# Kernel tuning notes

Hardware: AMD Instinct MI355X
Metric: run time of the kernel (lower is better)

Reference implementation:

```python
import jax, jax.numpy as jnp
import numpy as np

B, S, R, H, NH, HD = 32, 1026, 256, 1024, 16, 64

def setup_inputs() -> dict:
    key = jax.random.key(0)
    ks = jax.random.split(key, 8)
    sc = 0.02
    return {
        "q_low": jax.random.normal(ks[0], (B, S, R), jnp.float32),
        "k_low": jax.random.normal(ks[1], (B, S, R), jnp.float32),
        "v_low": jax.random.normal(ks[2], (B, S, R), jnp.float32),
        "Wq": jax.random.normal(ks[3], (R, H), jnp.float32) * sc,
        "bq": jnp.zeros((H,), jnp.float32),
        "Wk": jax.random.normal(ks[4], (R, H), jnp.float32) * sc,
        "bk": jnp.zeros((H,), jnp.float32),
        "Wv": jax.random.normal(ks[5], (R, H), jnp.float32) * sc,
        "bv": jnp.zeros((H,), jnp.float32),
        "Wo_down": jax.random.normal(ks[6], (H, R), jnp.float32) * sc,
    }

def reference(q_low, k_low, v_low, Wq, bq, Wk, bk, Wv, bv, Wo_down):
    # Up-project low-rank activations to full Q, K, V: [B,S,R] @ [R,H] -> [B,S,H]
    q = q_low @ Wq + bq
    k = k_low @ Wk + bk
    v = v_low @ Wv + bv
    # split heads: [B,S,NH,HD] -> [B,NH,S,HD]
    def split(x):
        return x.reshape(B, S, NH, HD).transpose(0, 2, 1, 3)
    qh, kh, vh = split(q), split(k), split(v)
    scores = jnp.einsum('bhqd,bhkd->bhqk', qh, kh) / jnp.sqrt(jnp.float32(HD))
    probs = jax.nn.softmax(scores, axis=-1)  # dropout p=0
    ctx = jnp.einsum('bhqk,bhkd->bhqd', probs, vh)
    ctx = ctx.transpose(0, 2, 1, 3).reshape(B, S, H)
    # Down-project with low-rank activation (gelu)
    out_low = jax.nn.gelu(ctx @ Wo_down, approximate=False)
    return out_low
```

## Files before the change

kernel.cpp:

```cpp
#include <hip/hip_runtime.h>
#include <hip/hip_bf16.h>
#include <math.h>

using short8   = __attribute__((ext_vector_type(8))) short;
using floatx4  = __attribute__((ext_vector_type(4))) float;
using floatx16 = __attribute__((ext_vector_type(16))) float;

#define B_N  32
#define S_N  1026
#define R_N  256
#define H_N  1024
#define NH_N 16
#define HD_N 64
#define SP_N 1088
#define KTILES 17

__device__ __forceinline__ float bf2f(__hip_bfloat16 x) { return __bfloat162float(x); }
__device__ __forceinline__ __hip_bfloat16 f2bf(float x) { return __float2bfloat16(x); }

__device__ __forceinline__ float fast_exp2(float x) {
#if __has_builtin(__builtin_amdgcn_exp2f)
    return __builtin_amdgcn_exp2f(x);
#else
    return exp2f(x);
#endif
}

__device__ __forceinline__ unsigned cvtpk(float lo, float hi_) {
    unsigned r;
    asm("v_cvt_pk_bf16_f32 %0, %1, %2" : "=v"(r) : "v"(lo), "v"(hi_));
    return r;
}

__device__ __forceinline__ void gl_lds16(const void* g, void* l) {
    __builtin_amdgcn_global_load_lds(
        (const __attribute__((address_space(1))) unsigned int*)g,
        (__attribute__((address_space(3))) unsigned int*)l, 16, 0, 0);
}

__device__ __forceinline__ int xcd_swz(int o, int nwg) {
    return ((nwg & 7) == 0) ? ((o & 7) * (nwg >> 3) + (o >> 3)) : o;
}

__device__ __forceinline__ short8 cvt8(const float* __restrict__ p) {
    floatx4 a = *(const floatx4*)p;
    floatx4 b = *(const floatx4*)(p + 4);
    short8 o;
    __hip_bfloat16* op = (__hip_bfloat16*)&o;
    op[0] = f2bf(a[0]); op[1] = f2bf(a[1]); op[2] = f2bf(a[2]); op[3] = f2bf(a[3]);
    op[4] = f2bf(b[0]); op[5] = f2bf(b[1]); op[6] = f2bf(b[2]); op[7] = f2bf(b[3]);
    return o;
}

__global__ __launch_bounds__(256) void transpose3_kernel(
    const float* __restrict__ a, const float* __restrict__ b, const float* __restrict__ c,
    __hip_bfloat16* __restrict__ oa, __hip_bfloat16* __restrict__ ob,
    __hip_bfloat16* __restrict__ oc, int K, int N) {
    __shared__ __hip_bfloat16 t[32][33];
    const float* in = (blockIdx.z == 0) ? a : (blockIdx.z == 1) ? b : c;
    __hip_bfloat16* out = (blockIdx.z == 0) ? oa : (blockIdx.z == 1) ? ob : oc;
    const int k0 = blockIdx.x * 32, n0 = blockIdx.y * 32;
    const int tx = threadIdx.x & 31, ty = threadIdx.x >> 5;
#pragma unroll
    for (int j = 0; j < 32; j += 8)
        t[ty + j][tx] = f2bf(in[(size_t)(k0 + ty + j) * N + n0 + tx]);
    __syncthreads();
#pragma unroll
    for (int j = 0; j < 32; j += 8)
        out[(size_t)(n0 + ty + j) * K + k0 + tx] = t[tx][ty + j];
}

__global__ __launch_bounds__(256) void transpose_kernel(const float* __restrict__ in,
                                                        __hip_bfloat16* __restrict__ out,
                                                        int K, int N) {
    __shared__ __hip_bfloat16 t[32][33];
    const int k0 = blockIdx.x * 32, n0 = blockIdx.y * 32;
    const int tx = threadIdx.x & 31, ty = threadIdx.x >> 5;
#pragma unroll
    for (int j = 0; j < 32; j += 8)
        t[ty + j][tx] = f2bf(in[(size_t)(k0 + ty + j) * N + n0 + tx]);
    __syncthreads();
#pragma unroll
    for (int j = 0; j < 32; j += 8)
        out[(size_t)(n0 + ty + j) * K + k0 + tx] = t[tx][ty + j];
}

__global__ __launch_bounds__(256) void cvtx_kernel(
    const float* __restrict__ q, const float* __restrict__ k, const float* __restrict__ v,
    __hip_bfloat16* __restrict__ oq, __hip_bfloat16* __restrict__ ok,
    __hip_bfloat16* __restrict__ ov, int n8) {
    int idx = blockIdx.x * 256 + threadIdx.x;
    if (idx >= n8) return;
    const float* s = (blockIdx.y == 0) ? q : (blockIdx.y == 1) ? k : v;
    __hip_bfloat16* d = (blockIdx.y == 0) ? oq : (blockIdx.y == 1) ? ok : ov;
    *(short8*)(d + (size_t)idx * 8) = cvt8(s + (size_t)idx * 8);
}

__global__ void padv_kernel(__hip_bfloat16* __restrict__ Vt, int total) {
    int idx = blockIdx.x * 256 + threadIdx.x;
    if (idx < total) {
        int p  = idx % (SP_N - S_N);
        int rd = idx / (SP_N - S_N);
        Vt[(size_t)rd * SP_N + S_N + p] = f2bf(0.f);
    }
}

__global__ __launch_bounds__(256) void qkvproj_kernel(
    const __hip_bfloat16* __restrict__ Xq, const __hip_bfloat16* __restrict__ Xk,
    const __hip_bfloat16* __restrict__ Xv,
    const __hip_bfloat16* __restrict__ WqT, const __hip_bfloat16* __restrict__ WkT,
    const __hip_bfloat16* __restrict__ WvT,
    const float* __restrict__ bq, const float* __restrict__ bk,
    const float* __restrict__ bv,
    __hip_bfloat16* __restrict__ Qc, __hip_bfloat16* __restrict__ Kc,
    __hip_bfloat16* __restrict__ Vc, int Mc, float qscale) {
    __shared__ __hip_bfloat16 As[2][128][64];
    __shared__ __hip_bfloat16 Bs[2][128][64];

    const int nx = gridDim.x;
    const int nwg = nx * 8 * 3;
    const int o = blockIdx.x + nx * (blockIdx.y + 8 * blockIdx.z);
    const int tlin = xcd_swz(o, nwg);
    const int ty = tlin & 7;
    const int rest = tlin >> 3;
    const int tx = rest % nx, tz = rest / nx;

    const __hip_bfloat16* X  = (tz == 0) ? Xq  : (tz == 1) ? Xk  : Xv;
    const __hip_bfloat16* WT = (tz == 0) ? WqT : (tz == 1) ? WkT : WvT;
    const float* bias        = (tz == 0) ? bq  : (tz == 1) ? bk  : bv;
    __hip_bfloat16* out      = (tz == 0) ? Qc  : (tz == 1) ? Kc  : Vc;
    const float oscale = (tz == 0) ? qscale : 1.0f;
    const int mode = (tz == 2);

    const int tid  = threadIdx.x;
    const int wave = tid >> 6, lane = tid & 63;
    const int quad = lane >> 4, l16 = lane & 15;
    const int tm = tx * 128, tn = ty * 128;
    const int mw = (wave >> 1) * 64, nw = (wave & 1) * 64;
    const int lr = lane >> 3;
    const int sc = (lane & 7) ^ lr;

    floatx4 acc[4][4] = {};

    auto stage = [&](int bb, int kk) {
#pragma unroll
        for (int s8 = 0; s8 < 4; ++s8) {
            int row = wave * 32 + s8 * 8;
            int gm = tm + row + lr; if (gm >= Mc) gm = Mc - 1;
            gl_lds16(X + (size_t)gm * R_N + kk + sc * 8, &As[bb][row][0]);
            gl_lds16(WT + (size_t)(tn + row + lr) * R_N + kk + sc * 8, &Bs[bb][row][0]);
        }
    };

    stage(0, 0);
    __syncthreads();

    for (int t = 0; t < R_N / 64; ++t) {
        const int bb = t & 1;
        if (t + 1 < R_N / 64) stage(bb ^ 1, (t + 1) * 64);
        short8 af[4][2], bfr[4][2];
#pragma unroll
        for (int mb = 0; mb < 4; ++mb) {
            int row = mw + mb * 16 + l16;
            const char* rp = (const char*)&As[bb][row][0];
#pragma unroll
            for (int k2 = 0; k2 < 2; ++k2)
                af[mb][k2] = *(const short8*)(rp + ((((k2 * 4 + quad)) ^ (row & 7)) << 4));
        }
#pragma unroll
        for (int nb = 0; nb < 4; ++nb) {
            int row = nw + nb * 16 + l16;
            const char* rp = (const char*)&Bs[bb][row][0];
#pragma unroll
            for (int k2 = 0; k2 < 2; ++k2)
                bfr[nb][k2] = *(const short8*)(rp + ((((k2 * 4 + quad)) ^ (row & 7)) << 4));
        }
        if (mode == 0) {
#pragma unroll
            for (int mb = 0; mb < 4; ++mb)
#pragma unroll
                for (int nb = 0; nb < 4; ++nb) {
                    acc[mb][nb] = __builtin_amdgcn_mfma_f32_16x16x32_bf16(af[mb][0], bfr[nb][0], acc[mb][nb], 0, 0, 0);
                    acc[mb][nb] = __builtin_amdgcn_mfma_f32_16x16x32_bf16(af[mb][1], bfr[nb][1], acc[mb][nb], 0, 0, 0);
                }
        } else {
#pragma unroll
            for (int mb = 0; mb < 4; ++mb)
#pragma unroll
                for (int nb = 0; nb < 4; ++nb) {
                    acc[mb][nb] = __builtin_amdgcn_mfma_f32_16x16x32_bf16(bfr[nb][0], af[mb][0], acc[mb][nb], 0, 0, 0);
                    acc[mb][nb] = __builtin_amdgcn_mfma_f32_16x16x32_bf16(bfr[nb][1], af[mb][1], acc[mb][nb], 0, 0, 0);
                }
        }
        __syncthreads();
    }

#pragma unroll
    for (int mb = 0; mb < 4; ++mb)
#pragma unroll
        for (int nb = 0; nb < 4; ++nb)
#pragma unroll
            for (int r = 0; r < 4; ++r) {
                int m, n;
                if (mode == 0) { m = tm + mw + mb * 16 + quad * 4 + r; n = tn + nw + nb * 16 + l16; }
                else           { n = tn + nw + nb * 16 + quad * 4 + r; m = tm + mw + mb * 16 + l16; }
                if (m >= Mc) continue;
                float v = oscale * (acc[mb][nb][r] + bias[n]);
                int bl = m / S_N, s = m - bl * S_N;
                int h = n >> 6, d = n & 63;
                size_t off = (mode == 0)
                    ? ((size_t)((bl * NH_N + h) * S_N + s)) * HD_N + d
                    : ((size_t)((bl * NH_N + h) * HD_N + d)) * SP_N + s;
                out[off] = f2bf(v);
            }
}

__global__ __launch_bounds__(256, 3) void attn_kernel(
    const __hip_bfloat16* __restrict__ Qh,
    const __hip_bfloat16* __restrict__ Kh,
    const __hip_bfloat16* __restrict__ Vt,
    __hip_bfloat16* __restrict__ ctx) {
    __shared__ __hip_bfloat16 Kl[2][64][64];
    __shared__ __hip_bfloat16 Vl[2][64][64];

    const int ny = gridDim.y;
    const int nwg = gridDim.x * ny;
    const int o = blockIdx.x + gridDim.x * blockIdx.y;
    const int tlin = xcd_swz(o, nwg);
    const int bh = tlin / ny;
    const int q0 = (tlin % ny) * 128;

    const int tid = threadIdx.x;
    const int wave = tid >> 6, lane = tid & 63;
    const int c = lane & 31, hi = lane >> 5, c7 = c & 7;
    const size_t base  = (size_t)bh * S_N * HD_N;
    const size_t vbase = (size_t)bh * HD_N * SP_N;

    const int lr = lane >> 3;
    const int sc = (lane & 7) ^ lr;

    short8 qf[4];
    {
        int qrow = q0 + wave * 32 + c;
        if (qrow > S_N - 1) qrow = S_N - 1;
        const __hip_bfloat16* qp = Qh + base + (size_t)qrow * HD_N + hi * 8;
#pragma unroll
        for (int i = 0; i < 4; ++i) qf[i] = *(const short8*)(qp + 16 * i);
    }

    floatx16 oacc[2] = {};
    float lsum = 0.f;

    auto stage = [&](int bb, int kt) {
#pragma unroll
        for (int j = 0; j < 2; ++j) {
            int r = 16 * wave + 8 * j + lr;
            int krow = kt + r;
            if (krow > S_N - 1) krow = S_N - 1;
            gl_lds16(Kh + base + (size_t)krow * HD_N + sc * 8,
                     &Kl[bb][16 * wave + 8 * j][0]);
            gl_lds16(Vt + vbase + (size_t)r * SP_N + kt + sc * 8,
                     &Vl[bb][16 * wave + 8 * j][0]);
        }
    };

    stage(0, 0);
    __syncthreads();

    int bb = 0;
    for (int t = 0; t < KTILES; ++t) {
        const int kt = t * 64;
        if (t + 1 < KTILES) stage(bb ^ 1, kt + 64);
        const bool last = (kt + 64 > S_N);

        short8 pa[2][2];
#pragma unroll
        for (int sub = 0; sub < 2; ++sub) {
            floatx16 sacc = {};
            __builtin_amdgcn_s_setprio(1);
#pragma unroll
            for (int i = 0; i < 4; ++i) {
                short8 kf = *(const short8*)&Kl[bb][32 * sub + c][(((2 * i + hi) ^ c7) << 3)];
                sacc = __builtin_amdgcn_mfma_f32_32x32x16_bf16(kf, qf[i], sacc, 0, 0, 0);
            }
            __builtin_amdgcn_s_setprio(0);
            float ps[16];
            if (!last) {
#pragma unroll
                for (int r = 0; r < 16; ++r) ps[r] = fast_exp2(sacc[r]);
            } else {
#pragma unroll
                for (int r = 0; r < 16; ++r) {
                    int key = kt + 32 * sub + (r & 3) + 8 * (r >> 2) + 4 * hi;
                    ps[r] = (key < S_N) ? fast_exp2(sacc[r]) : 0.f;
                }
            }
#pragma unroll
            for (int r = 0; r < 16; ++r) lsum += ps[r];
#pragma unroll
            for (int step = 0; step < 2; ++step) {
                unsigned w0 = cvtpk(ps[8 * step + 0], ps[8 * step + 1]);
                unsigned w1 = cvtpk(ps[8 * step + 2], ps[8 * step + 3]);
                unsigned w2 = cvtpk(ps[8 * step + 4], ps[8 * step + 5]);
                unsigned w3 = cvtpk(ps[8 * step + 6], ps[8 * step + 7]);
                asm("v_permlane32_swap_b32 %0, %1" : "+v"(w0), "+v"(w2));
                asm("v_permlane32_swap_b32 %0, %1" : "+v"(w1), "+v"(w3));
                union { unsigned u[4]; short8 s; } fu;
                fu.u[0] = w0; fu.u[1] = w1; fu.u[2] = w2; fu.u[3] = w3;
                pa[sub][step] = fu.s;
            }
        }

        __builtin_amdgcn_s_setprio(1);
#pragma unroll
        for (int db = 0; db < 2; ++db)
#pragma unroll
            for (int sub = 0; sub < 2; ++sub)
#pragma unroll
                for (int step = 0; step < 2; ++step) {
                    short8 vf = *(const short8*)
                        &Vl[bb][32 * db + c][((((sub * 2 + step) * 2 + hi) ^ c7) << 3)];
                    oacc[db] = __builtin_amdgcn_mfma_f32_32x32x16_bf16(pa[sub][step], vf, oacc[db], 0, 0, 0);
                }
        __builtin_amdgcn_s_setprio(0);

        __syncthreads();
        bb ^= 1;
    }

    lsum += __shfl_xor(lsum, 32);
    float rs = 1.0f / lsum;

    const int bl = bh / NH_N, h = bh - bl * NH_N;
    const int srow0 = q0 + wave * 32;
#pragma unroll
    for (int r = 0; r < 16; ++r) {
        int q = (r & 3) + 8 * (r >> 2) + 4 * hi;
        float rr = __shfl(rs, q, 32);
        int s = srow0 + q;
        if (s < S_N) {
            size_t o2 = ((size_t)(bl * S_N + s)) * H_N + h * HD_N + c;
            ctx[o2]      = f2bf(oacc[0][r] * rr);
            ctx[o2 + 32] = f2bf(oacc[1][r] * rr);
        }
    }
}

__global__ __launch_bounds__(256) void dproj_kernel(
    const __hip_bfloat16* __restrict__ X,
    const __hip_bfloat16* __restrict__ WT,
    float* __restrict__ out,
    int Mc) {
    __shared__ __hip_bfloat16 As[2][64][64];
    __shared__ __hip_bfloat16 Bs[2][128][64];

    const int tx = blockIdx.x, ty = blockIdx.y;

    const int tid  = threadIdx.x;
    const int wave = tid >> 6, lane = tid & 63;
    const int quad = lane >> 4, l16 = lane & 15;
    const int tm = tx * 64, tn = ty * 128;
    const int mw = (wave >> 1) * 32, nw = (wave & 1) * 64;
    const int lr = lane >> 3;
    const int sc = (lane & 7) ^ lr;

    floatx4 acc[2][4] = {};

    auto stage = [&](int bb, int kk) {
#pragma unroll
        for (int s8 = 0; s8 < 2; ++s8) {
            int row = wave * 16 + s8 * 8;
            int gm = tm + row + lr; if (gm >= Mc) gm = Mc - 1;
            gl_lds16(X + (size_t)gm * H_N + kk + sc * 8, &As[bb][row][0]);
        }
#pragma unroll
        for (int s8 = 0; s8 < 4; ++s8) {
            int row = wave * 32 + s8 * 8;
            gl_lds16(WT + (size_t)(tn + row + lr) * H_N + kk + sc * 8, &Bs[bb][row][0]);
        }
    };

    stage(0, 0);
    __syncthreads();

    for (int t = 0; t < H_N / 64; ++t) {
        const int bb = t & 1;
        if (t + 1 < H_N / 64) stage(bb ^ 1, (t + 1) * 64);
        short8 af[2][2], bfr[4][2];
#pragma unroll
        for (int mb = 0; mb < 2; ++mb) {
            int row = mw + mb * 16 + l16;
            const char* rp = (const char*)&As[bb][row][0];
#pragma unroll
            for (int k2 = 0; k2 < 2; ++k2)
                af[mb][k2] = *(const short8*)(rp + ((((k2 * 4 + quad)) ^ (row & 7)) << 4));
        }
#pragma unroll
        for (int nb = 0; nb < 4; ++nb) {
            int row = nw + nb * 16 + l16;
            const char* rp = (const char*)&Bs[bb][row][0];
#pragma unroll
            for (int k2 = 0; k2 < 2; ++k2)
                bfr[nb][k2] = *(const short8*)(rp + ((((k2 * 4 + quad)) ^ (row & 7)) << 4));
        }
#pragma unroll
        for (int mb = 0; mb < 2; ++mb)
#pragma unroll
            for (int nb = 0; nb < 4; ++nb) {
                acc[mb][nb] = __builtin_amdgcn_mfma_f32_16x16x32_bf16(af[mb][0], bfr[nb][0], acc[mb][nb], 0, 0, 0);
                acc[mb][nb] = __builtin_amdgcn_mfma_f32_16x16x32_bf16(af[mb][1], bfr[nb][1], acc[mb][nb], 0, 0, 0);
            }
        __syncthreads();
    }

#pragma unroll
    for (int mb = 0; mb < 2; ++mb)
#pragma unroll
        for (int nb = 0; nb < 4; ++nb)
#pragma unroll
            for (int r = 0; r < 4; ++r) {
                int m = tm + mw + mb * 16 + quad * 4 + r;
                int n = tn + nw + nb * 16 + l16;
                if (m >= Mc) continue;
                float x = acc[mb][nb][r];
                float g = 0.5f * x * (1.0f + erff(x * 0.70710678118654752f));
                out[(size_t)m * R_N + n] = g;
            }
}

extern "C" void kernel_launch(void* const* d_in, const int* in_sizes, int n_in,
                              void* d_out, int out_size, void* d_ws, size_t ws_size,
                              hipStream_t stream) {
    const float* q_low = (const float*)d_in[0];
    const float* k_low = (const float*)d_in[1];
    const float* v_low = (const float*)d_in[2];
    const float* Wq    = (const float*)d_in[3];
    const float* bq    = (const float*)d_in[4];
    const float* Wk    = (const float*)d_in[5];
    const float* bk    = (const float*)d_in[6];
    const float* Wv    = (const float*)d_in[7];
    const float* bv    = (const float*)d_in[8];
    const float* Wo    = (const float*)d_in[9];
    float* out = (float*)d_out;
    (void)in_sizes; (void)n_in; (void)out_size;

    const float QSCALE = 0.125f * 1.44269504088896f;
    const size_t SZ_W = (size_t)H_N * R_N * 2;

    int C = 32;
    while (C > 1) {
        size_t qk = (size_t)C * NH_N * S_N * HD_N * 2;
        size_t vv = (size_t)C * NH_N * HD_N * SP_N * 2;
        size_t cx = (size_t)C * S_N * H_N * 2;
        if (4 * SZ_W + 2 * qk + vv + cx <= ws_size) break;
        C >>= 1;
    }

    char* ws = (char*)d_ws;
    const size_t SZ_QK = (size_t)C * NH_N * S_N * HD_N * 2;
    const size_t SZ_V  = (size_t)C * NH_N * HD_N * SP_N * 2;
    __hip_bfloat16* WqT = (__hip_bfloat16*)(ws);
    __hip_bfloat16* WkT = (__hip_bfloat16*)(ws + SZ_W);
    __hip_bfloat16* WvT = (__hip_bfloat16*)(ws + 2 * SZ_W);
    __hip_bfloat16* WoT = (__hip_bfloat16*)(ws + 3 * SZ_W);
    __hip_bfloat16* Qc  = (__hip_bfloat16*)(ws + 4 * SZ_W);
    __hip_bfloat16* Kc  = (__hip_bfloat16*)(ws + 4 * SZ_W + SZ_QK);
    __hip_bfloat16* Vc  = (__hip_bfloat16*)(ws + 4 * SZ_W + 2 * SZ_QK);
    __hip_bfloat16* ctc = (__hip_bfloat16*)(ws + 4 * SZ_W + 2 * SZ_QK + SZ_V);

    {
        dim3 tg(R_N / 32, H_N / 32, 3);
        transpose3_kernel<<<tg, 256, 0, stream>>>(Wq, Wk, Wv, WqT, WkT, WvT, R_N, H_N);
        dim3 to(H_N / 32, R_N / 32);
        transpose_kernel<<<to, 256, 0, stream>>>(Wo, WoT, H_N, R_N);
    }

    {
        int total = C * NH_N * HD_N * (SP_N - S_N);
        padv_kernel<<<(total + 255) / 256, 256, 0, stream>>>(Vc, total);
    }

    for (int c0 = 0; c0 < B_N; c0 += C) {
        const int Mc = C * S_N;
        const size_t xoff = (size_t)c0 * S_N * R_N;

        __hip_bfloat16* Xq = ctc;
        __hip_bfloat16* Xk = ctc + (size_t)Mc * R_N;
        __hip_bfloat16* Xv = ctc + 2 * (size_t)Mc * R_N;
        {
            int n8 = Mc * R_N / 8;
            dim3 cg((n8 + 255) / 256, 3);
            cvtx_kernel<<<cg, 256, 0, stream>>>(q_low + xoff, k_low + xoff, v_low + xoff,
                                                Xq, Xk, Xv, n8);
        }

        dim3 pg((Mc + 127) / 128, H_N / 128, 3);
        qkvproj_kernel<<<pg, 256, 0, stream>>>(Xq, Xk, Xv, WqT, WkT, WvT,
                                               bq, bk, bv, Qc, Kc, Vc, Mc, QSCALE);

        dim3 ag(C * NH_N, (S_N + 127) / 128);
        attn_kernel<<<ag, 256, 0, stream>>>(Qc, Kc, Vc, ctc);

        dim3 dg((Mc + 63) / 64, R_N / 128);
        dproj_kernel<<<dg, 256, 0, stream>>>(ctc, WoT, out + xoff, Mc);
    }
}
```

Before: 559.7 us.

## Stage GEMM epilogues through LDS for coalesced vectorized global stores

The QKV projection and down-projection epilogues now write their accumulator tiles into shared memory, which reuses the operand staging buffers. Each thread then copies contiguous rows out to global memory with 16-byte or 4-byte vector stores, where before it issued scattered 2-byte or 4-byte stores. This targets poor write coalescing, which is worst for the transposed V layout and the per-head Q/K layout. In exchange it adds an extra LDS round trip and a barrier, and the shared-memory footprint in qkvproj is unchanged at 64KB.

```diff
diff --git a/kernel.cpp b/kernel.cpp
--- a/kernel.cpp
+++ b/kernel.cpp
@@ -14,6 +14,7 @@
 #define HD_N 64
 #define SP_N 1088
 #define KTILES 17
+#define CS_LD 136
 
 __device__ __forceinline__ float bf2f(__hip_bfloat16 x) { return __bfloat162float(x); }
 __device__ __forceinline__ __hip_bfloat16 f2bf(float x) { return __float2bfloat16(x); }
@@ -114,8 +115,11 @@
     const float* __restrict__ bv,
     __hip_bfloat16* __restrict__ Qc, __hip_bfloat16* __restrict__ Kc,
     __hip_bfloat16* __restrict__ Vc, int Mc, float qscale) {
-    __shared__ __hip_bfloat16 As[2][128][64];
-    __shared__ __hip_bfloat16 Bs[2][128][64];
+    __shared__ char smem[65536];
+    typedef __hip_bfloat16 (*AB_t)[128][64];
+    AB_t As = (AB_t)smem;
+    AB_t Bs = (AB_t)(smem + 32768);
+    __hip_bfloat16* Cs = (__hip_bfloat16*)smem;
 
     const int nx = gridDim.x;
     const int nwg = nx * 8 * 3;
@@ -195,24 +199,72 @@
         __syncthreads();
     }
 
-#pragma unroll
-    for (int mb = 0; mb < 4; ++mb)
-#pragma unroll
-        for (int nb = 0; nb < 4; ++nb)
-#pragma unroll
-            for (int r = 0; r < 4; ++r) {
-                int m, n;
-                if (mode == 0) { m = tm + mw + mb * 16 + quad * 4 + r; n = tn + nw + nb * 16 + l16; }
-                else           { n = tn + nw + nb * 16 + quad * 4 + r; m = tm + mw + mb * 16 + l16; }
-                if (m >= Mc) continue;
-                float v = oscale * (acc[mb][nb][r] + bias[n]);
-                int bl = m / S_N, s = m - bl * S_N;
-                int h = n >> 6, d = n & 63;
-                size_t off = (mode == 0)
-                    ? ((size_t)((bl * NH_N + h) * S_N + s)) * HD_N + d
-                    : ((size_t)((bl * NH_N + h) * HD_N + d)) * SP_N + s;
-                out[off] = f2bf(v);
-            }
+    if (mode == 0) {
+#pragma unroll
+        for (int mb = 0; mb < 4; ++mb)
+#pragma unroll
+            for (int nb = 0; nb < 4; ++nb) {
+                int j = nw + nb * 16 + l16;
+                float bv_ = bias[tn + j];
+#pragma unroll
+                for (int r = 0; r < 4; ++r) {
+                    int i = mw + mb * 16 + quad * 4 + r;
+                    Cs[i * CS_LD + j] = f2bf(oscale * (acc[mb][nb][r] + bv_));
+                }
+            }
+    } else {
+#pragma unroll
+        for (int mb = 0; mb < 4; ++mb)
+#pragma unroll
+            for (int nb = 0; nb < 4; ++nb)
+#pragma unroll
+                for (int r = 0; r < 4; ++r) {
+                    int i = nw + nb * 16 + quad * 4 + r;
+                    int j = mw + mb * 16 + l16;
+                    Cs[i * CS_LD + j] = f2bf(acc[mb][nb][r] + bias[tn + i]);
+                }
+    }
+    __syncthreads();
+
+    const int i = tid >> 1, half = tid & 1;
+    if (mode == 0) {
+        int m = tm + i;
+        if (m < Mc) {
+            int bl = m / S_N, s = m - bl * S_N;
+            int h = (tn >> 6) + half;
+            size_t ob = ((size_t)((bl * NH_N + h) * S_N + s)) * HD_N;
+            const __hip_bfloat16* src = Cs + i * CS_LD + half * 64;
+#pragma unroll
+            for (int j = 0; j < 8; ++j)
+                *(short8*)(out + ob + j * 8) = *(const short8*)(src + j * 8);
+        }
+    } else {
+        int n = tn + i;
+        int h = n >> 6, d = n & 63;
+        const __hip_bfloat16* src = Cs + i * CS_LD + half * 64;
+#pragma unroll
+        for (int j = 0; j < 8; ++j) {
+            int m0 = tm + half * 64 + j * 8;
+            if (m0 >= Mc) continue;
+            short8 w = *(const short8*)(src + j * 8);
+            int bl = m0 / S_N, s0 = m0 - bl * S_N;
+            size_t ob = ((size_t)((bl * NH_N + h) * HD_N + d)) * SP_N;
+            if (s0 + 8 <= S_N) {
+                const unsigned* wp = (const unsigned*)&w;
+#pragma unroll
+                for (int k = 0; k < 4; ++k)
+                    *(unsigned*)(out + ob + s0 + 2 * k) = wp[k];
+            } else {
+                const __hip_bfloat16* we = (const __hip_bfloat16*)&w;
+#pragma unroll
+                for (int e = 0; e < 8; ++e) {
+                    int m = m0 + e;
+                    int bl2 = m / S_N, s2 = m - bl2 * S_N;
+                    out[((size_t)((bl2 * NH_N + h) * HD_N + d)) * SP_N + s2] = we[e];
+                }
+            }
+        }
+    }
 }
 
 __global__ __launch_bounds__(256, 3) void attn_kernel(
@@ -351,8 +403,12 @@
     const __hip_bfloat16* __restrict__ WT,
     float* __restrict__ out,
     int Mc) {
-    __shared__ __hip_bfloat16 As[2][64][64];
-    __shared__ __hip_bfloat16 Bs[2][128][64];
+    __shared__ char smem[49152];
+    typedef __hip_bfloat16 (*A_t)[64][64];
+    typedef __hip_bfloat16 (*B_t)[128][64];
+    A_t As = (A_t)smem;
+    B_t Bs = (B_t)(smem + 16384);
+    float* Csf = (float*)smem;
 
     const int tx = blockIdx.x, ty = blockIdx.y;
 
@@ -419,13 +475,24 @@
         for (int nb = 0; nb < 4; ++nb)
 #pragma unroll
             for (int r = 0; r < 4; ++r) {
-                int m = tm + mw + mb * 16 + quad * 4 + r;
-                int n = tn + nw + nb * 16 + l16;
-                if (m >= Mc) continue;
+                int i = mw + mb * 16 + quad * 4 + r;
+                int j = nw + nb * 16 + l16;
                 float x = acc[mb][nb][r];
-                float g = 0.5f * x * (1.0f + erff(x * 0.70710678118654752f));
-                out[(size_t)m * R_N + n] = g;
-            }
+                Csf[i * CS_LD + j] = 0.5f * x * (1.0f + erff(x * 0.70710678118654752f));
+            }
+    __syncthreads();
+
+    {
+        const int i = tid >> 2, q32 = tid & 3;
+        int m = tm + i;
+        if (m < Mc) {
+            const float* src = Csf + i * CS_LD + q32 * 32;
+            float* dst = out + (size_t)m * R_N + tn + q32 * 32;
+#pragma unroll
+            for (int jj = 0; jj < 8; ++jj)
+                *(floatx4*)(dst + jj * 4) = *(const floatx4*)(src + jj * 4);
+        }
+    }
 }
 
 extern "C" void kernel_launch(void* const* d_in, const int* in_sizes, int n_in,
```

Measured after the change: 532.9 us. 4.8% less time.
